# Performance work log

Measured on AMD Instinct MI355X. Metric: run time of the kernel, lower is better.

The kernel has to match this reference:

```python
import jax, jax.numpy as jnp
import numpy as np

H = 16  # heads
DH = 64  # dim_head
SCALE = DH ** -0.5


def rotate_half(x):
    x1, x2 = jnp.split(x, 2, axis=-1)
    return jnp.concatenate([-x2, x1], axis=-1)


def apply_rope(pos, t):
    # pos: [n, d] broadcast over [b, h, n, d]
    return t * jnp.cos(pos) + rotate_half(t) * jnp.sin(pos)


def setup_inputs() -> dict:
    key = jax.random.key(0)
    ks = jax.random.split(key, 6)
    B, N, D = 4, 2048, 1024
    inner = H * DH
    x = jax.random.normal(ks[0], (B, N, D), dtype=jnp.float32)
    rotary_emb = jax.random.normal(ks[1], (N, DH), dtype=jnp.float32)
    Wq = jax.random.normal(ks[2], (D, inner), dtype=jnp.float32) / np.sqrt(D)
    Wkv = jax.random.normal(ks[3], (D, 2 * inner), dtype=jnp.float32) / np.sqrt(D)
    Wout = jax.random.normal(ks[4], (inner, D), dtype=jnp.float32) / np.sqrt(inner)
    bout = jnp.zeros((D,), dtype=jnp.float32)
    return {"x": x, "rotary_emb": rotary_emb, "Wq": Wq, "Wkv": Wkv, "Wout": Wout, "bout": bout}


def reference(x, rotary_emb, Wq, Wkv, Wout, bout):
    B, N, D = x.shape
    # QKV projections (self-attention: context = x)
    q = x @ Wq                       # [b, n, h*d]
    kv = x @ Wkv                     # [b, n, 2*h*d]
    k, v = jnp.split(kv, 2, axis=-1)

    def to_heads(t):
        return t.reshape(B, N, H, DH).transpose(0, 2, 1, 3)  # [b, h, n, d]

    q, k, v = to_heads(q), to_heads(k), to_heads(v)
    q = apply_rope(rotary_emb, q)
    k = apply_rope(rotary_emb, k)

    # scaled dot-product attention
    scores = jnp.einsum('bhid,bhjd->bhij', q, k) * SCALE
    attn = jax.nn.softmax(scores, axis=-1)
    out = jnp.einsum('bhij,bhjd->bhid', attn, v)  # [b, h, n, d]
    out = out.transpose(0, 2, 1, 3).reshape(B, N, H * DH)
    return out @ Wout + bout
```

## Files before the change

### kernel.cpp

```cpp
#include <hip/hip_runtime.h>

#define BB 4
#define NN 2048
#define DD 1024
#define HH 16
#define DHH 64
#define MM (BB*NN)
#define QS 3072

typedef unsigned short u16;
typedef __attribute__((ext_vector_type(8))) short short8;
typedef __attribute__((ext_vector_type(4))) float floatx4;

#if __has_builtin(__builtin_amdgcn_exp2f)
#define EXP2F __builtin_amdgcn_exp2f
#else
#define EXP2F exp2f
#endif

__device__ __forceinline__ u16 f2bf(float f) {
  union { float f; unsigned u; } v; v.f = f;
  unsigned u = v.u;
  return (u16)((u + 0x7fffu + ((u >> 16) & 1u)) >> 16);
}
__device__ __forceinline__ float bf2f(u16 h) {
  union { unsigned u; float f; } v; v.u = ((unsigned)h) << 16;
  return v.f;
}
__device__ __forceinline__ unsigned fbits(float f) {
  union { float f; unsigned u; } v; v.f = f; return v.u;
}
__device__ __forceinline__ unsigned pkbf(float lo, float hi) {
#if __has_builtin(__builtin_amdgcn_perm)
  return __builtin_amdgcn_perm(fbits(hi), fbits(lo), 0x07060302u);
#else
  return (fbits(lo) >> 16) | (fbits(hi) & 0xffff0000u);
#endif
}
__device__ __forceinline__ void gll16(const u16* g, u16* l) {
  __builtin_amdgcn_global_load_lds((const __attribute__((address_space(1))) unsigned int*)g,
                                   (__attribute__((address_space(3))) unsigned int*)l, 16, 0, 0);
}
__device__ __forceinline__ int toff(int row, int kc) {
  int pr = row >> 1;
  int c = (((row & 1) << 2) + kc) ^ (pr & 7);
  return pr * 64 + c * 8;
}

#define SOFTMAX_SCALE 0.18033688f
#define SOFTMAX_BIAS  -28.8539008f

__global__ __launch_bounds__(256) void prep_kernel(const float* __restrict__ x,
                                                   const float* __restrict__ rot,
                                                   const float* __restrict__ Wq,
                                                   const float* __restrict__ Wkv,
                                                   const float* __restrict__ Wout,
                                                   u16* __restrict__ xb,
                                                   u16* __restrict__ WT,
                                                   u16* __restrict__ WoutT,
                                                   float2* __restrict__ tab) {
  __shared__ float t[64][65];
  int bid = blockIdx.x;
  int tid = threadIdx.x;
  if (bid < 8192) {
    int i = (bid * 256 + tid) * 4;
    float4 v = *(const float4*)(x + i);
    u16 o[4] = {f2bf(v.x), f2bf(v.y), f2bf(v.z), f2bf(v.w)};
    *(uint2*)(xb + i) = *(uint2*)o;
  } else if (bid < 9216) {
    int r = bid - 8192;
    int bx = r & 63, by = r >> 6;
    const float* src;
    u16* dst;
    int C, c0;
    if (bx < 16)      { src = Wq;   dst = WT;                   C = 1024; c0 = bx * 64; }
    else if (bx < 48) { src = Wkv;  dst = WT + (size_t)DD * DD; C = 2048; c0 = (bx - 16) * 64; }
    else              { src = Wout; dst = WoutT;                C = 1024; c0 = (bx - 48) * 64; }
    const int R = 1024;
    int r0 = by * 64;
#pragma unroll
    for (int i = 0; i < 16; ++i) {
      int lin = i * 256 + tid;
      int rr = lin >> 6, cc = lin & 63;
      t[rr][cc] = src[(size_t)(r0 + rr) * C + c0 + cc];
    }
    __syncthreads();
#pragma unroll
    for (int i = 0; i < 16; ++i) {
      int lin = i * 256 + tid;
      int rr = lin >> 6, cc = lin & 63;
      dst[(size_t)(c0 + rr) * R + r0 + cc] = f2bf(t[cc][rr]);
    }
  } else {
    int i = (bid - 9216) * 256 + tid;
    int n = i >> 6, d = i & 63;
    float p = rot[i];
    float s, c;
    __sincosf(p, &s, &c);
    tab[(size_t)d * NN + n] = make_float2(c, s);
  }
}

__global__ __launch_bounds__(512, 2) void gemm_qk(const u16* __restrict__ A,
                                                  const u16* __restrict__ Bt,
                                                  u16* __restrict__ qd,
                                                  u16* __restrict__ kd,
                                                  const float2* __restrict__ tab) {
  const int K = DD;
  const int NT = K / 64;
  __shared__ __align__(16) u16 lds[65536];
  int tid = threadIdx.x;
  int wave = tid >> 6, lane = tid & 63;
  int q4 = lane >> 4, l16 = lane & 15;
  int wr = wave >> 2, wc = wave & 3;

  int flat = blockIdx.y * 8 + blockIdx.x;
  int wg = (flat & 7) * 32 + (flat >> 3);
  int bx = wg & 7, by = wg >> 3;
  int m0 = by * 256, n0 = bx * 256;

  const u16* Ag = A + (size_t)m0 * K;
  const u16* Bg = Bt + (size_t)n0 * K;

  int spr = tid >> 3, sct = tid & 7, su = sct ^ (spr & 7);
  int srow = spr * 2 + (su >> 2);
  int skc = (su & 3) * 8;
  size_t so = (size_t)srow * K + skc;

  int toffA[8], toffB[4];
#pragma unroll
  for (int mi = 0; mi < 8; ++mi) toffA[mi] = wr * 4096 + toff(mi * 16 + l16, q4);
#pragma unroll
  for (int ni = 0; ni < 4; ++ni)
    toffB[ni] = (wc >> 1) * 4096 + toff((wc & 1) * 64 + ni * 16 + l16, q4);

  floatx4 acc[8][4];
#pragma unroll
  for (int mi = 0; mi < 8; ++mi)
#pragma unroll
    for (int ni = 0; ni < 4; ++ni) acc[mi][ni] = (floatx4){0.f, 0.f, 0.f, 0.f};

  auto stageHalf = [&](int t, int mat, int kh) {
    const u16* src = (mat ? Bg : Ag) + so + t * 64 + kh * 32;
    u16* dst = lds + (t & 1) * 32768 + mat * 16384 + kh * 8192 + wave * 512;
    gll16(src, dst);
    gll16(src + (size_t)128 * K, dst + 4096);
  };

  stageHalf(0, 1, 0); stageHalf(0, 0, 0); stageHalf(0, 1, 1); stageHalf(0, 0, 1);
  stageHalf(1, 1, 0); stageHalf(1, 0, 0); stageHalf(1, 1, 1);
  __builtin_amdgcn_s_waitcnt(0x0F76);
  __builtin_amdgcn_s_barrier();

#pragma unroll
  for (int t = 0; t < NT; ++t) {
    const u16* Ab = lds + (t & 1) * 32768;
    const u16* Bb = Ab + 16384;
    short8 af[4], bfq[4];

#pragma unroll
    for (int ni = 0; ni < 4; ++ni) bfq[ni] = *(const short8*)(Bb + toffB[ni]);
#pragma unroll
    for (int f = 0; f < 4; ++f) af[f] = *(const short8*)(Ab + toffA[f]);
    if (t + 1 < NT) stageHalf(t + 1, 0, 1);
    __builtin_amdgcn_s_barrier();
    __builtin_amdgcn_s_waitcnt(0xC07F);
    __builtin_amdgcn_s_setprio(1);
#pragma unroll
    for (int f = 0; f < 4; ++f)
#pragma unroll
      for (int ni = 0; ni < 4; ++ni)
        acc[f][ni] = __builtin_amdgcn_mfma_f32_16x16x32_bf16(bfq[ni], af[f], acc[f][ni], 0, 0, 0);
    __builtin_amdgcn_s_setprio(0);
    __builtin_amdgcn_s_barrier();

#pragma unroll
    for (int f = 0; f < 4; ++f) af[f] = *(const short8*)(Ab + toffA[4 + f]);
    if (t + 2 < NT) stageHalf(t + 2, 1, 0);
    __builtin_amdgcn_s_barrier();
    __builtin_amdgcn_s_waitcnt(0xC07F);
    __builtin_amdgcn_s_setprio(1);
#pragma unroll
    for (int f = 0; f < 4; ++f)
#pragma unroll
      for (int ni = 0; ni < 4; ++ni)
        acc[4 + f][ni] = __builtin_amdgcn_mfma_f32_16x16x32_bf16(bfq[ni], af[f], acc[4 + f][ni], 0, 0, 0);
    __builtin_amdgcn_s_setprio(0);
    __builtin_amdgcn_s_barrier();

#pragma unroll
    for (int ni = 0; ni < 4; ++ni) bfq[ni] = *(const short8*)(Bb + 8192 + toffB[ni]);
#pragma unroll
    for (int f = 0; f < 4; ++f) af[f] = *(const short8*)(Ab + 8192 + toffA[f]);
    if (t + 2 < NT) stageHalf(t + 2, 0, 0);
    __builtin_amdgcn_s_barrier();
    __builtin_amdgcn_s_waitcnt(0xC07F);
    __builtin_amdgcn_s_setprio(1);
#pragma unroll
    for (int f = 0; f < 4; ++f)
#pragma unroll
      for (int ni = 0; ni < 4; ++ni)
        acc[f][ni] = __builtin_amdgcn_mfma_f32_16x16x32_bf16(bfq[ni], af[f], acc[f][ni], 0, 0, 0);
    __builtin_amdgcn_s_setprio(0);
    __builtin_amdgcn_s_barrier();

#pragma unroll
    for (int f = 0; f < 4; ++f) af[f] = *(const short8*)(Ab + 8192 + toffA[4 + f]);
    if (t + 2 < NT) stageHalf(t + 2, 1, 1);
    __builtin_amdgcn_s_barrier();
    __builtin_amdgcn_s_waitcnt(0xC07F);
    __builtin_amdgcn_s_setprio(1);
#pragma unroll
    for (int f = 0; f < 4; ++f)
#pragma unroll
      for (int ni = 0; ni < 4; ++ni)
        acc[4 + f][ni] = __builtin_amdgcn_mfma_f32_16x16x32_bf16(bfq[ni], af[f], acc[4 + f][ni], 0, 0, 0);
    __builtin_amdgcn_s_setprio(0);
    if (t == NT - 2) __builtin_amdgcn_s_waitcnt(0x0F70);
    else if (t < NT - 2) __builtin_amdgcn_s_waitcnt(0x0F76);
    __builtin_amdgcn_s_barrier();
  }

  int h = (n0 + wc * 64) >> 6;
  u16* dst = (h < 16) ? qd : kd;
  int hh = h & 15;
  float scl = (h < 16) ? SOFTMAX_SCALE : 1.0f;
  int b = m0 >> 11;
  int tokbase = (m0 & (NN - 1)) + wr * 128;
#pragma unroll
  for (int mi = 0; mi < 8; ++mi) {
    int tok = tokbase + mi * 16 + l16;
    u16* rowp = dst + ((size_t)(b * HH + hh) * NN + tok) * 64;
#pragma unroll
    for (int ni = 0; ni < 2; ++ni) {
      int d0 = ni * 16 + q4 * 4;
      u16 plo[4], phi[4];
#pragma unroll
      for (int r = 0; r < 4; ++r) {
        float2 cs0 = tab[(size_t)(d0 + r) * NN + tok];
        float2 cs1 = tab[(size_t)(d0 + r + 32) * NN + tok];
        float v0 = acc[mi][ni][r], v1 = acc[mi][ni + 2][r];
        plo[r] = f2bf((v0 * cs0.x - v1 * cs0.y) * scl);
        phi[r] = f2bf((v1 * cs1.x + v0 * cs1.y) * scl);
      }
      *(uint2*)(rowp + d0) = *(uint2*)plo;
      *(uint2*)(rowp + d0 + 32) = *(uint2*)phi;
    }
  }
}

__global__ __launch_bounds__(256) void gemm_v(const u16* __restrict__ A,
                                              const u16* __restrict__ Bt,
                                              u16* __restrict__ vt) {
  const int K = DD;
  __shared__ __align__(16) u16 lds[16384];
  int tid = threadIdx.x;
  int wave = tid >> 6, lane = tid & 63;
  int q4 = lane >> 4, l16 = lane & 15;

  int flat = blockIdx.y * 8 + blockIdx.x;
  int wg = (flat & 7) * 64 + (flat >> 3);
  int bx = wg & 7, by = wg >> 3;
  int m0 = by * 128, n0 = bx * 128;

  int wm = (wave >> 1) * 64, wn = (wave & 1) * 64;

  const u16* Ag = A + (size_t)m0 * K;
  const u16* Bg = Bt + (size_t)(2048 + n0) * K;
  int o1 = tid, o2 = tid + 256;
  int pr1 = o1 >> 3, c1 = (o1 & 7) ^ (pr1 & 7);
  int row1 = pr1 * 2 + (c1 >> 2), kc1 = (c1 & 3) * 8;
  int pr2 = o2 >> 3, c2 = (o2 & 7) ^ (pr2 & 7);
  int row2 = pr2 * 2 + (c2 >> 2), kc2 = (c2 & 3) * 8;
  int d1 = wave * 512, d2 = 2048 + wave * 512;

  int foA[4], foB[4];
#pragma unroll
  for (int i = 0; i < 4; ++i) {
    foA[i] = toff(wm + i * 16 + l16, q4);
    foB[i] = toff(wn + i * 16 + l16, q4);
  }

  floatx4 acc[4][4];
#pragma unroll
  for (int mi = 0; mi < 4; ++mi)
#pragma unroll
    for (int ni = 0; ni < 4; ++ni) acc[mi][ni] = (floatx4){0.f, 0.f, 0.f, 0.f};

  gll16(Ag + (size_t)row1 * K + kc1, lds + d1);
  gll16(Ag + (size_t)row2 * K + kc2, lds + d2);
  gll16(Bg + (size_t)row1 * K + kc1, lds + 8192 + d1);
  gll16(Bg + (size_t)row2 * K + kc2, lds + 8192 + d2);

  for (int k0 = 0, it = 0; k0 < K; k0 += 32, ++it) {
    int boff = (it & 1) * 4096;
    if (k0 + 32 < K) {
      int nboff = 4096 - boff;
      int kn = k0 + 32;
      gll16(Ag + (size_t)row1 * K + kn + kc1, lds + nboff + d1);
      gll16(Ag + (size_t)row2 * K + kn + kc2, lds + nboff + d2);
      gll16(Bg + (size_t)row1 * K + kn + kc1, lds + 8192 + nboff + d1);
      gll16(Bg + (size_t)row2 * K + kn + kc2, lds + 8192 + nboff + d2);
      __builtin_amdgcn_s_waitcnt(0x0F74);
    } else {
      __builtin_amdgcn_s_waitcnt(0x0F70);
    }
    __builtin_amdgcn_s_barrier();
    const u16* Ac = lds + boff;
    const u16* Bc = lds + 8192 + boff;
    short8 af[4], bfr[4];
#pragma unroll
    for (int i = 0; i < 4; ++i) {
      af[i]  = *(const short8*)(Ac + foA[i]);
      bfr[i] = *(const short8*)(Bc + foB[i]);
    }
#pragma unroll
    for (int mi = 0; mi < 4; ++mi)
#pragma unroll
      for (int ni = 0; ni < 4; ++ni)
        acc[mi][ni] = __builtin_amdgcn_mfma_f32_16x16x32_bf16(af[mi], bfr[ni], acc[mi][ni], 0, 0, 0);
    __builtin_amdgcn_s_barrier();
  }

  int h = (n0 + wn) >> 6;
#pragma unroll
  for (int mi = 0; mi < 4; ++mi) {
    int mbase = m0 + wm + mi * 16 + q4 * 4;
    int b = mbase >> 11;
    int nn = mbase & (NN - 1);
    u16* base = vt + (size_t)(b * HH + h) * (NN * 64) + (nn >> 6) * 4096 + (nn & 63);
#pragma unroll
    for (int ni = 0; ni < 4; ++ni) {
      int d = ni * 16 + l16;
      u16 p[4] = {f2bf(acc[mi][ni][0]), f2bf(acc[mi][ni][1]),
                  f2bf(acc[mi][ni][2]), f2bf(acc[mi][ni][3])};
      *(uint2*)(base + d * 64) = *(uint2*)p;
    }
  }
}

__global__ __launch_bounds__(256) void gemm_out(const u16* __restrict__ A,
                                                const u16* __restrict__ Bt,
                                                float* __restrict__ Cout,
                                                const float* __restrict__ bias,
                                                int M, int N, int K) {
  __shared__ __align__(16) u16 lds[16384];
  int tid = threadIdx.x;
  int wave = tid >> 6, lane = tid & 63;
  int q4 = lane >> 4, l16 = lane & 15;
  int m0 = blockIdx.y * 128, n0 = blockIdx.x * 128;
  int wm = (wave >> 1) * 64, wn = (wave & 1) * 64;

  const u16* Ag = A + (size_t)m0 * K;
  const u16* Bg = Bt + (size_t)n0 * K;
  int o1 = tid, o2 = tid + 256;
  int pr1 = o1 >> 3, c1 = (o1 & 7) ^ (pr1 & 7);
  int row1 = pr1 * 2 + (c1 >> 2), kc1 = (c1 & 3) * 8;
  int pr2 = o2 >> 3, c2 = (o2 & 7) ^ (pr2 & 7);
  int row2 = pr2 * 2 + (c2 >> 2), kc2 = (c2 & 3) * 8;
  int d1 = wave * 512, d2 = 2048 + wave * 512;

  int foA[4], foB[4];
#pragma unroll
  for (int i = 0; i < 4; ++i) {
    foA[i] = toff(wm + i * 16 + l16, q4);
    foB[i] = toff(wn + i * 16 + l16, q4);
  }

  floatx4 acc[4][4];
#pragma unroll
  for (int mi = 0; mi < 4; ++mi)
#pragma unroll
    for (int ni = 0; ni < 4; ++ni) acc[mi][ni] = (floatx4){0.f, 0.f, 0.f, 0.f};

  gll16(Ag + (size_t)row1 * K + kc1, lds + d1);
  gll16(Ag + (size_t)row2 * K + kc2, lds + d2);
  gll16(Bg + (size_t)row1 * K + kc1, lds + 8192 + d1);
  gll16(Bg + (size_t)row2 * K + kc2, lds + 8192 + d2);

  for (int k0 = 0, it = 0; k0 < K; k0 += 32, ++it) {
    int boff = (it & 1) * 4096;
    if (k0 + 32 < K) {
      int nboff = 4096 - boff;
      int kn = k0 + 32;
      gll16(Ag + (size_t)row1 * K + kn + kc1, lds + nboff + d1);
      gll16(Ag + (size_t)row2 * K + kn + kc2, lds + nboff + d2);
      gll16(Bg + (size_t)row1 * K + kn + kc1, lds + 8192 + nboff + d1);
      gll16(Bg + (size_t)row2 * K + kn + kc2, lds + 8192 + nboff + d2);
      __builtin_amdgcn_s_waitcnt(0x0F74);
    } else {
      __builtin_amdgcn_s_waitcnt(0x0F70);
    }
    __builtin_amdgcn_s_barrier();
    const u16* Ac = lds + boff;
    const u16* Bc = lds + 8192 + boff;
    short8 af[4], bfr[4];
#pragma unroll
    for (int i = 0; i < 4; ++i) {
      af[i]  = *(const short8*)(Ac + foA[i]);
      bfr[i] = *(const short8*)(Bc + foB[i]);
    }
#pragma unroll
    for (int mi = 0; mi < 4; ++mi)
#pragma unroll
      for (int ni = 0; ni < 4; ++ni)
        acc[mi][ni] = __builtin_amdgcn_mfma_f32_16x16x32_bf16(af[mi], bfr[ni], acc[mi][ni], 0, 0, 0);
    __builtin_amdgcn_s_barrier();
  }

#pragma unroll
  for (int ni = 0; ni < 4; ++ni) {
    int col = n0 + wn + ni * 16 + l16;
    float bval = bias[col];
#pragma unroll
    for (int mi = 0; mi < 4; ++mi) {
#pragma unroll
      for (int r = 0; r < 4; ++r) {
        int row = m0 + wm + mi * 16 + q4 * 4 + r;
        Cout[(size_t)row * N + col] = acc[mi][ni][r] + bval;
      }
    }
  }
}

__global__ __launch_bounds__(512, 2) void attn_kernel(const u16* __restrict__ qd,
                                                      const u16* __restrict__ kd,
                                                      const u16* __restrict__ vt,
                                                      u16* __restrict__ ao) {
  __shared__ __align__(16) u16 lds[32768];

  int tid = threadIdx.x, wave = tid >> 6, lane = tid & 63;
  int q4 = lane >> 4, l16 = lane & 15;

  int F = blockIdx.y * 4 + blockIdx.x;
  int xcd = F & 7, r = F >> 3;
  int bh = xcd * 8 + (r >> 2);
  int qt = r & 3;
  int b = bh >> 4, h = bh & 15;

  const u16* qbh = qd + (size_t)bh * NN * 64;
  const u16* kbh = kd + (size_t)bh * NN * 64;
  const u16* vbh = vt + (size_t)bh * NN * 64;

  int srow = wave * 8 + (lane >> 3);
  int g = ((lane & 7) ^ ((lane >> 3) & 7)) * 8;
  int prow = ((srow >> 2) & 3) * 8 + ((srow >> 4) & 1) * 4 + (srow & 3) + ((srow >> 5) & 1) * 32;

#pragma unroll
  for (int it = 0; it < 8; ++it)
    gll16(qbh + (size_t)(qt * 512 + it * 64 + srow) * 64 + g, lds + (it * 64 + wave * 8) * 64);
  __builtin_amdgcn_s_waitcnt(0x0F70);
  __builtin_amdgcn_s_barrier();

  short8 aq[4][2];
#pragma unroll
  for (int mi = 0; mi < 4; ++mi)
#pragma unroll
    for (int ks = 0; ks < 2; ++ks) {
      int row = wave * 64 + mi * 16 + l16;
      aq[mi][ks] = *(const short8*)(lds + row * 64 + (((ks * 4 + q4) ^ (row & 7)) * 8));
    }
  __builtin_amdgcn_s_waitcnt(0xC07F);
  __builtin_amdgcn_s_barrier();

  auto stageKV = [&](int t) {
    gll16(kbh + (size_t)(t * 64 + prow) * 64 + g, lds + (t & 3) * 4096 + wave * 512);
    gll16(vbh + (size_t)t * 4096 + srow * 64 + g, lds + 16384 + (t & 3) * 4096 + wave * 512);
  };
  stageKV(0); stageKV(1);

  union { unsigned u[4]; short8 s8; } ones;
#pragma unroll
  for (int i = 0; i < 4; ++i) ones.u[i] = 0x3F803F80u;

  const floatx4 biasc = (floatx4){SOFTMAX_BIAS, SOFTMAX_BIAS, SOFTMAX_BIAS, SOFTMAX_BIAS};

  floatx4 lacc[4];
  floatx4 o[4][4];
#pragma unroll
  for (int mi = 0; mi < 4; ++mi) {
    lacc[mi] = (floatx4){0.f, 0.f, 0.f, 0.f};
#pragma unroll
    for (int di = 0; di < 4; ++di) o[mi][di] = (floatx4){0.f, 0.f, 0.f, 0.f};
  }

  auto TILE = [&](int t) {
    const u16* Kc = lds + (t & 3) * 4096;
    const u16* Vc = lds + 16384 + (t & 3) * 4096;

    floatx4 s[4][4];
    {
      short8 kf[4];
#pragma unroll
      for (int kg = 0; kg < 4; ++kg) {
        int row = kg * 16 + l16;
        kf[kg] = *(const short8*)(Kc + row * 64 + ((q4 ^ (row & 7)) * 8));
      }
      __builtin_amdgcn_s_setprio(1);
#pragma unroll
      for (int kg = 0; kg < 4; ++kg)
#pragma unroll
        for (int mi = 0; mi < 4; ++mi)
          s[kg][mi] = __builtin_amdgcn_mfma_f32_16x16x32_bf16(kf[kg], aq[mi][0], biasc, 0, 0, 0);
      __builtin_amdgcn_s_setprio(0);
    }
    {
      short8 kf[4];
#pragma unroll
      for (int kg = 0; kg < 4; ++kg) {
        int row = kg * 16 + l16;
        kf[kg] = *(const short8*)(Kc + row * 64 + (((4 + q4) ^ (row & 7)) * 8));
      }
      __builtin_amdgcn_s_setprio(1);
#pragma unroll
      for (int kg = 0; kg < 4; ++kg)
#pragma unroll
        for (int mi = 0; mi < 4; ++mi)
          s[kg][mi] = __builtin_amdgcn_mfma_f32_16x16x32_bf16(kf[kg], aq[mi][1], s[kg][mi], 0, 0, 0);
      __builtin_amdgcn_s_setprio(0);
    }

    unsigned pk[4][4][2];
#pragma unroll
    for (int kg = 0; kg < 4; ++kg)
#pragma unroll
      for (int mi = 0; mi < 4; ++mi) {
        float e0 = EXP2F(s[kg][mi][0]);
        float e1 = EXP2F(s[kg][mi][1]);
        float e2 = EXP2F(s[kg][mi][2]);
        float e3 = EXP2F(s[kg][mi][3]);
        pk[kg][mi][0] = pkbf(e0, e1);
        pk[kg][mi][1] = pkbf(e2, e3);
      }

#pragma unroll
    for (int ks = 0; ks < 2; ++ks) {
      short8 vf[4];
#pragma unroll
      for (int di = 0; di < 4; ++di) {
        int row = di * 16 + l16;
        vf[di] = *(const short8*)(Vc + row * 64 + (((ks * 4 + q4) ^ (row & 7)) * 8));
      }
      __builtin_amdgcn_s_setprio(1);
#pragma unroll
      for (int mi = 0; mi < 4; ++mi) {
        union { unsigned u[4]; short8 s8; } bw;
        bw.u[0] = pk[2 * ks][mi][0];
        bw.u[1] = pk[2 * ks][mi][1];
        bw.u[2] = pk[2 * ks + 1][mi][0];
        bw.u[3] = pk[2 * ks + 1][mi][1];
        lacc[mi] = __builtin_amdgcn_mfma_f32_16x16x32_bf16(ones.s8, bw.s8, lacc[mi], 0, 0, 0);
#pragma unroll
        for (int di = 0; di < 4; ++di)
          o[mi][di] = __builtin_amdgcn_mfma_f32_16x16x32_bf16(vf[di], bw.s8, o[mi][di], 0, 0, 0);
      }
      __builtin_amdgcn_s_setprio(0);
    }
  };

  const int NT = NN / 64;

  for (int j = 0; j < NT / 2; ++j) {
    int t0 = 2 * j;
    __builtin_amdgcn_s_waitcnt(0x0F70);
    __builtin_amdgcn_s_barrier();
    if (t0 + 2 < NT) { stageKV(t0 + 2); stageKV(t0 + 3); }
    TILE(t0);
    TILE(t0 + 1);
  }

#pragma unroll
  for (int mi = 0; mi < 4; ++mi) {
    float rinv = 1.0f / lacc[mi][0];
    int qrow = qt * 512 + wave * 64 + mi * 16 + l16;
    size_t base = (size_t)(b * NN + qrow) * DD + h * DHH + q4 * 4;
#pragma unroll
    for (int di = 0; di < 4; ++di) {
      u16 p[4] = {f2bf(o[mi][di][0] * rinv), f2bf(o[mi][di][1] * rinv),
                  f2bf(o[mi][di][2] * rinv), f2bf(o[mi][di][3] * rinv)};
      *(uint2*)(ao + base + di * 16) = *(uint2*)p;
    }
  }
}

extern "C" void kernel_launch(void* const* d_in, const int* in_sizes, int n_in,
                              void* d_out, int out_size, void* d_ws, size_t ws_size,
                              hipStream_t stream) {
  const float* x    = (const float*)d_in[0];
  const float* rot  = (const float*)d_in[1];
  const float* Wq   = (const float*)d_in[2];
  const float* Wkv  = (const float*)d_in[3];
  const float* Wout = (const float*)d_in[4];
  const float* bout = (const float*)d_in[5];
  float* out = (float*)d_out;

  char* ws = (char*)d_ws;
  size_t off = 0;
  auto alloc = [&](size_t bytes) {
    void* p = ws + off;
    off = (off + bytes + 255) & ~(size_t)255;
    return p;
  };
  u16*    xb    = (u16*)alloc((size_t)MM * DD * 2);
  u16*    WT    = (u16*)alloc((size_t)QS * DD * 2);
  u16*    WoutT = (u16*)alloc((size_t)DD * DD * 2);
  float2* tab   = (float2*)alloc((size_t)NN * DHH * 8);
  u16*    qdb   = (u16*)alloc((size_t)MM * DD * 2);
  u16*    kdb   = (u16*)alloc((size_t)MM * DD * 2);
  u16*    vtt   = (u16*)alloc((size_t)MM * DD * 2);
  u16*    ao    = (u16*)alloc((size_t)MM * DD * 2);

  prep_kernel<<<9728, 256, 0, stream>>>(x, rot, Wq, Wkv, Wout, xb, WT, WoutT, tab);

  gemm_qk<<<dim3(8, 32), 512, 0, stream>>>(xb, WT, qdb, kdb, tab);
  gemm_v<<<dim3(8, 64), 256, 0, stream>>>(xb, WT, vtt);

  attn_kernel<<<dim3(NN / 512, BB * HH), 512, 0, stream>>>(qdb, kdb, vtt, ao);

  gemm_out<<<dim3(DD / 128, MM / 128), 256, 0, stream>>>(ao, WoutT, out, bout, MM, DD, DD);
}
```

Before: 260.1 us.

## Merge Q/K and V projection GEMMs into one 256x256-tile launch

Replaces the separate gemm_qk and gemm_v kernels with one gemm_qkv launch of 384 workgroups. The first 256 blocks do the Q/K tiles with the RoPE epilogue and the remaining 128 do the V tiles, using the same 256x256 pipelined MFMA schedule. V blocks swap the MFMA operand order so their output lands in the transposed V layout. The RoPE table is now stored token-major, so epilogue reads are contiguous per token. The goal is to remove one launch and give V the larger, better-pipelined tile. The cost is duplicated code and a larger branch-heavy kernel.

```diff
diff --git a/kernel.cpp b/kernel.cpp
--- a/kernel.cpp
+++ b/kernel.cpp
@@ -93,19 +93,19 @@
     }
   } else {
     int i = (bid - 9216) * 256 + tid;
-    int n = i >> 6, d = i & 63;
     float p = rot[i];
     float s, c;
     __sincosf(p, &s, &c);
-    tab[(size_t)d * NN + n] = make_float2(c, s);
-  }
-}
-
-__global__ __launch_bounds__(512, 2) void gemm_qk(const u16* __restrict__ A,
-                                                  const u16* __restrict__ Bt,
-                                                  u16* __restrict__ qd,
-                                                  u16* __restrict__ kd,
-                                                  const float2* __restrict__ tab) {
+    tab[i] = make_float2(c, s);
+  }
+}
+
+__global__ __launch_bounds__(512, 2) void gemm_qkv(const u16* __restrict__ A,
+                                                   const u16* __restrict__ Bt,
+                                                   u16* __restrict__ qd,
+                                                   u16* __restrict__ kd,
+                                                   u16* __restrict__ vt,
+                                                   const float2* __restrict__ tab) {
   const int K = DD;
   const int NT = K / 64;
   __shared__ __align__(16) u16 lds[65536];
@@ -114,10 +114,12 @@
   int q4 = lane >> 4, l16 = lane & 15;
   int wr = wave >> 2, wc = wave & 3;
 
-  int flat = blockIdx.y * 8 + blockIdx.x;
-  int wg = (flat & 7) * 32 + (flat >> 3);
-  int bx = wg & 7, by = wg >> 3;
-  int m0 = by * 256, n0 = bx * 256;
+  int flat = blockIdx.x;
+  int wg = (flat & 7) * 48 + (flat >> 3);
+  bool isv = wg >= 256;
+  int m0, n0;
+  if (!isv) { m0 = (wg >> 3) * 256; n0 = (wg & 7) * 256; }
+  else      { int r = wg - 256; m0 = (r >> 2) * 256; n0 = 2048 + (r & 3) * 256; }
 
   const u16* Ag = A + (size_t)m0 * K;
   const u16* Bg = Bt + (size_t)n0 * K;
@@ -133,12 +135,6 @@
 #pragma unroll
   for (int ni = 0; ni < 4; ++ni)
     toffB[ni] = (wc >> 1) * 4096 + toff((wc & 1) * 64 + ni * 16 + l16, q4);
-
-  floatx4 acc[8][4];
-#pragma unroll
-  for (int mi = 0; mi < 8; ++mi)
-#pragma unroll
-    for (int ni = 0; ni < 4; ++ni) acc[mi][ni] = (floatx4){0.f, 0.f, 0.f, 0.f};
 
   auto stageHalf = [&](int t, int mat, int kh) {
     const u16* src = (mat ? Bg : Ag) + so + t * 64 + kh * 32;
@@ -152,189 +148,200 @@
   __builtin_amdgcn_s_waitcnt(0x0F76);
   __builtin_amdgcn_s_barrier();
 
-#pragma unroll
-  for (int t = 0; t < NT; ++t) {
-    const u16* Ab = lds + (t & 1) * 32768;
-    const u16* Bb = Ab + 16384;
-    short8 af[4], bfq[4];
-
-#pragma unroll
-    for (int ni = 0; ni < 4; ++ni) bfq[ni] = *(const short8*)(Bb + toffB[ni]);
-#pragma unroll
-    for (int f = 0; f < 4; ++f) af[f] = *(const short8*)(Ab + toffA[f]);
-    if (t + 1 < NT) stageHalf(t + 1, 0, 1);
-    __builtin_amdgcn_s_barrier();
-    __builtin_amdgcn_s_waitcnt(0xC07F);
-    __builtin_amdgcn_s_setprio(1);
-#pragma unroll
-    for (int f = 0; f < 4; ++f)
-#pragma unroll
-      for (int ni = 0; ni < 4; ++ni)
-        acc[f][ni] = __builtin_amdgcn_mfma_f32_16x16x32_bf16(bfq[ni], af[f], acc[f][ni], 0, 0, 0);
-    __builtin_amdgcn_s_setprio(0);
-    __builtin_amdgcn_s_barrier();
-
-#pragma unroll
-    for (int f = 0; f < 4; ++f) af[f] = *(const short8*)(Ab + toffA[4 + f]);
-    if (t + 2 < NT) stageHalf(t + 2, 1, 0);
-    __builtin_amdgcn_s_barrier();
-    __builtin_amdgcn_s_waitcnt(0xC07F);
-    __builtin_amdgcn_s_setprio(1);
-#pragma unroll
-    for (int f = 0; f < 4; ++f)
-#pragma unroll
-      for (int ni = 0; ni < 4; ++ni)
-        acc[4 + f][ni] = __builtin_amdgcn_mfma_f32_16x16x32_bf16(bfq[ni], af[f], acc[4 + f][ni], 0, 0, 0);
-    __builtin_amdgcn_s_setprio(0);
-    __builtin_amdgcn_s_barrier();
-
-#pragma unroll
-    for (int ni = 0; ni < 4; ++ni) bfq[ni] = *(const short8*)(Bb + 8192 + toffB[ni]);
-#pragma unroll
-    for (int f = 0; f < 4; ++f) af[f] = *(const short8*)(Ab + 8192 + toffA[f]);
-    if (t + 2 < NT) stageHalf(t + 2, 0, 0);
-    __builtin_amdgcn_s_barrier();
-    __builtin_amdgcn_s_waitcnt(0xC07F);
-    __builtin_amdgcn_s_setprio(1);
-#pragma unroll
-    for (int f = 0; f < 4; ++f)
-#pragma unroll
-      for (int ni = 0; ni < 4; ++ni)
-        acc[f][ni] = __builtin_amdgcn_mfma_f32_16x16x32_bf16(bfq[ni], af[f], acc[f][ni], 0, 0, 0);
-    __builtin_amdgcn_s_setprio(0);
-    __builtin_amdgcn_s_barrier();
-
-#pragma unroll
-    for (int f = 0; f < 4; ++f) af[f] = *(const short8*)(Ab + 8192 + toffA[4 + f]);
-    if (t + 2 < NT) stageHalf(t + 2, 1, 1);
-    __builtin_amdgcn_s_barrier();
-    __builtin_amdgcn_s_waitcnt(0xC07F);
-    __builtin_amdgcn_s_setprio(1);
-#pragma unroll
-    for (int f = 0; f < 4; ++f)
-#pragma unroll
-      for (int ni = 0; ni < 4; ++ni)
-        acc[4 + f][ni] = __builtin_amdgcn_mfma_f32_16x16x32_bf16(bfq[ni], af[f], acc[4 + f][ni], 0, 0, 0);
-    __builtin_amdgcn_s_setprio(0);
-    if (t == NT - 2) __builtin_amdgcn_s_waitcnt(0x0F70);
-    else if (t < NT - 2) __builtin_amdgcn_s_waitcnt(0x0F76);
-    __builtin_amdgcn_s_barrier();
-  }
-
-  int h = (n0 + wc * 64) >> 6;
-  u16* dst = (h < 16) ? qd : kd;
-  int hh = h & 15;
-  float scl = (h < 16) ? SOFTMAX_SCALE : 1.0f;
-  int b = m0 >> 11;
-  int tokbase = (m0 & (NN - 1)) + wr * 128;
-#pragma unroll
-  for (int mi = 0; mi < 8; ++mi) {
-    int tok = tokbase + mi * 16 + l16;
-    u16* rowp = dst + ((size_t)(b * HH + hh) * NN + tok) * 64;
-#pragma unroll
-    for (int ni = 0; ni < 2; ++ni) {
-      int d0 = ni * 16 + q4 * 4;
-      u16 plo[4], phi[4];
-#pragma unroll
-      for (int r = 0; r < 4; ++r) {
-        float2 cs0 = tab[(size_t)(d0 + r) * NN + tok];
-        float2 cs1 = tab[(size_t)(d0 + r + 32) * NN + tok];
-        float v0 = acc[mi][ni][r], v1 = acc[mi][ni + 2][r];
-        plo[r] = f2bf((v0 * cs0.x - v1 * cs0.y) * scl);
-        phi[r] = f2bf((v1 * cs1.x + v0 * cs1.y) * scl);
-      }
-      *(uint2*)(rowp + d0) = *(uint2*)plo;
-      *(uint2*)(rowp + d0 + 32) = *(uint2*)phi;
-    }
-  }
-}
-
-__global__ __launch_bounds__(256) void gemm_v(const u16* __restrict__ A,
-                                              const u16* __restrict__ Bt,
-                                              u16* __restrict__ vt) {
-  const int K = DD;
-  __shared__ __align__(16) u16 lds[16384];
-  int tid = threadIdx.x;
-  int wave = tid >> 6, lane = tid & 63;
-  int q4 = lane >> 4, l16 = lane & 15;
-
-  int flat = blockIdx.y * 8 + blockIdx.x;
-  int wg = (flat & 7) * 64 + (flat >> 3);
-  int bx = wg & 7, by = wg >> 3;
-  int m0 = by * 128, n0 = bx * 128;
-
-  int wm = (wave >> 1) * 64, wn = (wave & 1) * 64;
-
-  const u16* Ag = A + (size_t)m0 * K;
-  const u16* Bg = Bt + (size_t)(2048 + n0) * K;
-  int o1 = tid, o2 = tid + 256;
-  int pr1 = o1 >> 3, c1 = (o1 & 7) ^ (pr1 & 7);
-  int row1 = pr1 * 2 + (c1 >> 2), kc1 = (c1 & 3) * 8;
-  int pr2 = o2 >> 3, c2 = (o2 & 7) ^ (pr2 & 7);
-  int row2 = pr2 * 2 + (c2 >> 2), kc2 = (c2 & 3) * 8;
-  int d1 = wave * 512, d2 = 2048 + wave * 512;
-
-  int foA[4], foB[4];
-#pragma unroll
-  for (int i = 0; i < 4; ++i) {
-    foA[i] = toff(wm + i * 16 + l16, q4);
-    foB[i] = toff(wn + i * 16 + l16, q4);
-  }
-
-  floatx4 acc[4][4];
-#pragma unroll
-  for (int mi = 0; mi < 4; ++mi)
-#pragma unroll
-    for (int ni = 0; ni < 4; ++ni) acc[mi][ni] = (floatx4){0.f, 0.f, 0.f, 0.f};
-
-  gll16(Ag + (size_t)row1 * K + kc1, lds + d1);
-  gll16(Ag + (size_t)row2 * K + kc2, lds + d2);
-  gll16(Bg + (size_t)row1 * K + kc1, lds + 8192 + d1);
-  gll16(Bg + (size_t)row2 * K + kc2, lds + 8192 + d2);
-
-  for (int k0 = 0, it = 0; k0 < K; k0 += 32, ++it) {
-    int boff = (it & 1) * 4096;
-    if (k0 + 32 < K) {
-      int nboff = 4096 - boff;
-      int kn = k0 + 32;
-      gll16(Ag + (size_t)row1 * K + kn + kc1, lds + nboff + d1);
-      gll16(Ag + (size_t)row2 * K + kn + kc2, lds + nboff + d2);
-      gll16(Bg + (size_t)row1 * K + kn + kc1, lds + 8192 + nboff + d1);
-      gll16(Bg + (size_t)row2 * K + kn + kc2, lds + 8192 + nboff + d2);
-      __builtin_amdgcn_s_waitcnt(0x0F74);
-    } else {
-      __builtin_amdgcn_s_waitcnt(0x0F70);
-    }
-    __builtin_amdgcn_s_barrier();
-    const u16* Ac = lds + boff;
-    const u16* Bc = lds + 8192 + boff;
-    short8 af[4], bfr[4];
-#pragma unroll
-    for (int i = 0; i < 4; ++i) {
-      af[i]  = *(const short8*)(Ac + foA[i]);
-      bfr[i] = *(const short8*)(Bc + foB[i]);
-    }
-#pragma unroll
-    for (int mi = 0; mi < 4; ++mi)
-#pragma unroll
-      for (int ni = 0; ni < 4; ++ni)
-        acc[mi][ni] = __builtin_amdgcn_mfma_f32_16x16x32_bf16(af[mi], bfr[ni], acc[mi][ni], 0, 0, 0);
-    __builtin_amdgcn_s_barrier();
-  }
-
-  int h = (n0 + wn) >> 6;
-#pragma unroll
-  for (int mi = 0; mi < 4; ++mi) {
-    int mbase = m0 + wm + mi * 16 + q4 * 4;
-    int b = mbase >> 11;
-    int nn = mbase & (NN - 1);
-    u16* base = vt + (size_t)(b * HH + h) * (NN * 64) + (nn >> 6) * 4096 + (nn & 63);
-#pragma unroll
-    for (int ni = 0; ni < 4; ++ni) {
-      int d = ni * 16 + l16;
-      u16 p[4] = {f2bf(acc[mi][ni][0]), f2bf(acc[mi][ni][1]),
-                  f2bf(acc[mi][ni][2]), f2bf(acc[mi][ni][3])};
-      *(uint2*)(base + d * 64) = *(uint2*)p;
+  if (!isv) {
+    floatx4 acc[8][4];
+#pragma unroll
+    for (int mi = 0; mi < 8; ++mi)
+#pragma unroll
+      for (int ni = 0; ni < 4; ++ni) acc[mi][ni] = (floatx4){0.f, 0.f, 0.f, 0.f};
+
+#pragma unroll
+    for (int t = 0; t < NT; ++t) {
+      const u16* Ab = lds + (t & 1) * 32768;
+      const u16* Bb = Ab + 16384;
+      short8 af[4], bfq[4];
+
+#pragma unroll
+      for (int ni = 0; ni < 4; ++ni) bfq[ni] = *(const short8*)(Bb + toffB[ni]);
+#pragma unroll
+      for (int f = 0; f < 4; ++f) af[f] = *(const short8*)(Ab + toffA[f]);
+      if (t + 1 < NT) stageHalf(t + 1, 0, 1);
+      __builtin_amdgcn_s_barrier();
+      __builtin_amdgcn_s_waitcnt(0xC07F);
+      __builtin_amdgcn_s_setprio(1);
+#pragma unroll
+      for (int f = 0; f < 4; ++f)
+#pragma unroll
+        for (int ni = 0; ni < 4; ++ni)
+          acc[f][ni] = __builtin_amdgcn_mfma_f32_16x16x32_bf16(bfq[ni], af[f], acc[f][ni], 0, 0, 0);
+      __builtin_amdgcn_s_setprio(0);
+      __builtin_amdgcn_s_barrier();
+
+#pragma unroll
+      for (int f = 0; f < 4; ++f) af[f] = *(const short8*)(Ab + toffA[4 + f]);
+      if (t + 2 < NT) stageHalf(t + 2, 1, 0);
+      __builtin_amdgcn_s_barrier();
+      __builtin_amdgcn_s_waitcnt(0xC07F);
+      __builtin_amdgcn_s_setprio(1);
+#pragma unroll
+      for (int f = 0; f < 4; ++f)
+#pragma unroll
+        for (int ni = 0; ni < 4; ++ni)
+          acc[4 + f][ni] = __builtin_amdgcn_mfma_f32_16x16x32_bf16(bfq[ni], af[f], acc[4 + f][ni], 0, 0, 0);
+      __builtin_amdgcn_s_setprio(0);
+      __builtin_amdgcn_s_barrier();
+
+#pragma unroll
+      for (int ni = 0; ni < 4; ++ni) bfq[ni] = *(const short8*)(Bb + 8192 + toffB[ni]);
+#pragma unroll
+      for (int f = 0; f < 4; ++f) af[f] = *(const short8*)(Ab + 8192 + toffA[f]);
+      if (t + 2 < NT) stageHalf(t + 2, 0, 0);
+      __builtin_amdgcn_s_barrier();
+      __builtin_amdgcn_s_waitcnt(0xC07F);
+      __builtin_amdgcn_s_setprio(1);
+#pragma unroll
+      for (int f = 0; f < 4; ++f)
+#pragma unroll
+        for (int ni = 0; ni < 4; ++ni)
+          acc[f][ni] = __builtin_amdgcn_mfma_f32_16x16x32_bf16(bfq[ni], af[f], acc[f][ni], 0, 0, 0);
+      __builtin_amdgcn_s_setprio(0);
+      __builtin_amdgcn_s_barrier();
+
+#pragma unroll
+      for (int f = 0; f < 4; ++f) af[f] = *(const short8*)(Ab + 8192 + toffA[4 + f]);
+      if (t + 2 < NT) stageHalf(t + 2, 1, 1);
+      __builtin_amdgcn_s_barrier();
+      __builtin_amdgcn_s_waitcnt(0xC07F);
+      __builtin_amdgcn_s_setprio(1);
+#pragma unroll
+      for (int f = 0; f < 4; ++f)
+#pragma unroll
+        for (int ni = 0; ni < 4; ++ni)
+          acc[4 + f][ni] = __builtin_amdgcn_mfma_f32_16x16x32_bf16(bfq[ni], af[f], acc[4 + f][ni], 0, 0, 0);
+      __builtin_amdgcn_s_setprio(0);
+      if (t == NT - 2) __builtin_amdgcn_s_waitcnt(0x0F70);
+      else if (t < NT - 2) __builtin_amdgcn_s_waitcnt(0x0F76);
+      __builtin_amdgcn_s_barrier();
+    }
+
+    int h = (n0 + wc * 64) >> 6;
+    u16* dst = (h < 16) ? qd : kd;
+    int hh = h & 15;
+    float scl = (h < 16) ? SOFTMAX_SCALE : 1.0f;
+    int b = m0 >> 11;
+    int tokbase = (m0 & (NN - 1)) + wr * 128;
+#pragma unroll
+    for (int mi = 0; mi < 8; ++mi) {
+      int tok = tokbase + mi * 16 + l16;
+      u16* rowp = dst + ((size_t)(b * HH + hh) * NN + tok) * 64;
+      const float2* tb = tab + tok * 64;
+#pragma unroll
+      for (int ni = 0; ni < 2; ++ni) {
+        int d0 = ni * 16 + q4 * 4;
+        u16 plo[4], phi[4];
+#pragma unroll
+        for (int r = 0; r < 4; ++r) {
+          float2 cs0 = tb[d0 + r];
+          float2 cs1 = tb[d0 + r + 32];
+          float v0 = acc[mi][ni][r], v1 = acc[mi][ni + 2][r];
+          plo[r] = f2bf((v0 * cs0.x - v1 * cs0.y) * scl);
+          phi[r] = f2bf((v1 * cs1.x + v0 * cs1.y) * scl);
+        }
+        *(uint2*)(rowp + d0) = *(uint2*)plo;
+        *(uint2*)(rowp + d0 + 32) = *(uint2*)phi;
+      }
+    }
+  } else {
+    floatx4 acc[8][4];
+#pragma unroll
+    for (int mi = 0; mi < 8; ++mi)
+#pragma unroll
+      for (int ni = 0; ni < 4; ++ni) acc[mi][ni] = (floatx4){0.f, 0.f, 0.f, 0.f};
+
+#pragma unroll
+    for (int t = 0; t < NT; ++t) {
+      const u16* Ab = lds + (t & 1) * 32768;
+      const u16* Bb = Ab + 16384;
+      short8 af[4], bfq[4];
+
+#pragma unroll
+      for (int ni = 0; ni < 4; ++ni) bfq[ni] = *(const short8*)(Bb + toffB[ni]);
+#pragma unroll
+      for (int f = 0; f < 4; ++f) af[f] = *(const short8*)(Ab + toffA[f]);
+      if (t + 1 < NT) stageHalf(t + 1, 0, 1);
+      __builtin_amdgcn_s_barrier();
+      __builtin_amdgcn_s_waitcnt(0xC07F);
+      __builtin_amdgcn_s_setprio(1);
+#pragma unroll
+      for (int f = 0; f < 4; ++f)
+#pragma unroll
+        for (int ni = 0; ni < 4; ++ni)
+          acc[f][ni] = __builtin_amdgcn_mfma_f32_16x16x32_bf16(af[f], bfq[ni], acc[f][ni], 0, 0, 0);
+      __builtin_amdgcn_s_setprio(0);
+      __builtin_amdgcn_s_barrier();
+
+#pragma unroll
+      for (int f = 0; f < 4; ++f) af[f] = *(const short8*)(Ab + toffA[4 + f]);
+      if (t + 2 < NT) stageHalf(t + 2, 1, 0);
+      __builtin_amdgcn_s_barrier();
+      __builtin_amdgcn_s_waitcnt(0xC07F);
+      __builtin_amdgcn_s_setprio(1);
+#pragma unroll
+      for (int f = 0; f < 4; ++f)
+#pragma unroll
+        for (int ni = 0; ni < 4; ++ni)
+          acc[4 + f][ni] = __builtin_amdgcn_mfma_f32_16x16x32_bf16(af[f], bfq[ni], acc[4 + f][ni], 0, 0, 0);
+      __builtin_amdgcn_s_setprio(0);
+      __builtin_amdgcn_s_barrier();
+
+#pragma unroll
+      for (int ni = 0; ni < 4; ++ni) bfq[ni] = *(const short8*)(Bb + 8192 + toffB[ni]);
+#pragma unroll
+      for (int f = 0; f < 4; ++f) af[f] = *(const short8*)(Ab + 8192 + toffA[f]);
+      if (t + 2 < NT) stageHalf(t + 2, 0, 0);
+      __builtin_amdgcn_s_barrier();
+      __builtin_amdgcn_s_waitcnt(0xC07F);
+      __builtin_amdgcn_s_setprio(1);
+#pragma unroll
+      for (int f = 0; f < 4; ++f)
+#pragma unroll
+        for (int ni = 0; ni < 4; ++ni)
+          acc[f][ni] = __builtin_amdgcn_mfma_f32_16x16x32_bf16(af[f], bfq[ni], acc[f][ni], 0, 0, 0);
+      __builtin_amdgcn_s_setprio(0);
+      __builtin_amdgcn_s_barrier();
+
+#pragma unroll
+      for (int f = 0; f < 4; ++f) af[f] = *(const short8*)(Ab + 8192 + toffA[4 + f]);
+      if (t + 2 < NT) stageHalf(t + 2, 1, 1);
+      __builtin_amdgcn_s_barrier();
+      __builtin_amdgcn_s_waitcnt(0xC07F);
+      __builtin_amdgcn_s_setprio(1);
+#pragma unroll
+      for (int f = 0; f < 4; ++f)
+#pragma unroll
+        for (int ni = 0; ni < 4; ++ni)
+          acc[4 + f][ni] = __builtin_amdgcn_mfma_f32_16x16x32_bf16(af[f], bfq[ni], acc[4 + f][ni], 0, 0, 0);
+      __builtin_amdgcn_s_setprio(0);
+      if (t == NT - 2) __builtin_amdgcn_s_waitcnt(0x0F70);
+      else if (t < NT - 2) __builtin_amdgcn_s_waitcnt(0x0F76);
+      __builtin_amdgcn_s_barrier();
+    }
+
+    int vcol0 = (n0 - 2048) + (wc >> 1) * 128 + (wc & 1) * 64;
+#pragma unroll
+    for (int mi = 0; mi < 8; ++mi) {
+      int tokb = m0 + wr * 128 + mi * 16 + q4 * 4;
+      int b = tokb >> 11;
+      int nn = tokb & (NN - 1);
+#pragma unroll
+      for (int ni = 0; ni < 4; ++ni) {
+        int d = vcol0 + ni * 16 + l16;
+        int h = d >> 6, dd = d & 63;
+        u16 p[4] = {f2bf(acc[mi][ni][0]), f2bf(acc[mi][ni][1]),
+                    f2bf(acc[mi][ni][2]), f2bf(acc[mi][ni][3])};
+        *(uint2*)(vt + (size_t)(b * HH + h) * (NN * 64) + (nn >> 6) * 4096 + dd * 64 + (nn & 63)) =
+            *(uint2*)p;
+      }
     }
   }
 }
@@ -612,8 +619,7 @@
 
   prep_kernel<<<9728, 256, 0, stream>>>(x, rot, Wq, Wkv, Wout, xb, WT, WoutT, tab);
 
-  gemm_qk<<<dim3(8, 32), 512, 0, stream>>>(xb, WT, qdb, kdb, tab);
-  gemm_v<<<dim3(8, 64), 256, 0, stream>>>(xb, WT, vtt);
+  gemm_qkv<<<dim3(384), 512, 0, stream>>>(xb, WT, qdb, kdb, vtt, tab);
 
   attn_kernel<<<dim3(NN / 512, BB * HH), 512, 0, stream>>>(qdb, kdb, vtt, ao);
 
```

After: 269.0 us. 1.03x slower.
